# Kernel optimization log

Measured on AMD Instinct MI355X. Metric: run time of the kernel, lower is better.

Reference implementation:

```python
import jax, jax.numpy as jnp
import numpy as np

D_MODEL = 1024
NUM_HEAD = 16
D_K = D_MODEL // NUM_HEAD


def setup_inputs() -> dict:
    key = jax.random.key(0)
    ks = jax.random.split(key, 9)
    s = 1.0 / np.sqrt(D_MODEL)
    x = jax.random.normal(ks[0], (2, 2048, D_MODEL), dtype=jnp.float32)
    Wq = jax.random.uniform(ks[1], (D_MODEL, D_MODEL), jnp.float32, -s, s)
    bq = jax.random.uniform(ks[2], (D_MODEL,), jnp.float32, -s, s)
    Wk = jax.random.uniform(ks[3], (D_MODEL, D_MODEL), jnp.float32, -s, s)
    bk = jax.random.uniform(ks[4], (D_MODEL,), jnp.float32, -s, s)
    Wv = jax.random.uniform(ks[5], (D_MODEL, D_MODEL), jnp.float32, -s, s)
    bv = jax.random.uniform(ks[6], (D_MODEL,), jnp.float32, -s, s)
    Wo = jax.random.uniform(ks[7], (D_MODEL, D_MODEL), jnp.float32, -s, s)
    bo = jax.random.uniform(ks[8], (D_MODEL,), jnp.float32, -s, s)
    return {"x": x, "Wq": Wq, "bq": bq, "Wk": Wk, "bk": bk,
            "Wv": Wv, "bv": bv, "Wo": Wo, "bo": bo}


def reference(x, Wq, bq, Wk, bk, Wv, bv, Wo, bo):
    b, n, d = x.shape
    h, dk = NUM_HEAD, D_K
    # Linear projections (torch Linear: x @ W.T + b)
    q = (x @ Wq.T + bq).reshape(b, n, h, dk).transpose(0, 2, 1, 3)  # [b,h,n,dk]
    k = (x @ Wk.T + bk).reshape(b, n, h, dk).transpose(0, 2, 1, 3)
    v = (x @ Wv.T + bv).reshape(b, n, h, dk).transpose(0, 2, 1, 3)
    scores = jnp.einsum('bhqd,bhkd->bhqk', q, k) / jnp.sqrt(jnp.float32(dk))
    attn = jax.nn.softmax(scores, axis=-1)  # [b,h,n,n]
    out = jnp.einsum('bhqk,bhkd->bhqd', attn, v)
    out = out.transpose(0, 2, 1, 3).reshape(b, n, d)
    return out @ Wo.T + bo
```

## Files before the change

kernel.cpp:

```cpp
#include <hip/hip_runtime.h>

#define BATCH   2
#define SEQ     2048
#define DMODEL  1024
#define NHEAD   16
#define DKH     64
#define MTOT    (BATCH*SEQ)
#define KDIM    DMODEL

#define XB    0u
#define WQB   (4u*1024u*1024u)
#define WKB   (5u*1024u*1024u)
#define WVB   (6u*1024u*1024u)
#define WOB   (7u*1024u*1024u)
#define QOFF  (8u*1024u*1024u)
#define KOFF  (12u*1024u*1024u)
#define VOFF  (16u*1024u*1024u)
#define OOFF  (20u*1024u*1024u)

typedef __bf16 bf16x8 __attribute__((ext_vector_type(8)));
typedef __bf16 bf16x4 __attribute__((ext_vector_type(4)));
typedef float  f32x4  __attribute__((ext_vector_type(4)));
typedef float  f32x16 __attribute__((ext_vector_type(16)));

__device__ __forceinline__ void async16(const __bf16* g, __bf16* l) {
  __builtin_amdgcn_global_load_lds(
      (const __attribute__((address_space(1))) void*)g,
      (__attribute__((address_space(3))) void*)l, 16, 0, 0);
}

#define VWAIT(N) asm volatile("s_waitcnt vmcnt(" #N ")" ::: "memory")

__device__ __forceinline__ unsigned cvtpk_bf16(float lo, float hi) {
  unsigned r;
  asm("v_cvt_pk_bf16_f32 %0, %1, %2" : "=v"(r) : "v"(lo), "v"(hi));
  return r;
}
__device__ __forceinline__ void plswap(unsigned& a, unsigned& b) {
  asm("v_permlane32_swap_b32 %0, %1" : "+v"(a), "+v"(b));
}

__global__ __launch_bounds__(256) void cvt_fp32_bf16(
    const float* __restrict__ x,  const float* __restrict__ wq,
    const float* __restrict__ wk, const float* __restrict__ wv,
    const float* __restrict__ wo, __bf16* __restrict__ ws)
{
  const float* src; __bf16* dst; int n;
  switch (blockIdx.y) {
    case 0:  src = x;  dst = ws + XB;  n = 4 * 1024 * 1024; break;
    case 1:  src = wq; dst = ws + WQB; n = 1024 * 1024;     break;
    case 2:  src = wk; dst = ws + WKB; n = 1024 * 1024;     break;
    case 3:  src = wv; dst = ws + WVB; n = 1024 * 1024;     break;
    default: src = wo; dst = ws + WOB; n = 1024 * 1024;     break;
  }
  const int i = (blockIdx.x * 256 + threadIdx.x) * 8;
  if (i < n) {
    const float4 a = *(const float4*)(src + i);
    const float4 b = *(const float4*)(src + i + 4);
    bf16x8 o;
    o[0] = (__bf16)a.x; o[1] = (__bf16)a.y; o[2] = (__bf16)a.z; o[3] = (__bf16)a.w;
    o[4] = (__bf16)b.x; o[5] = (__bf16)b.y; o[6] = (__bf16)b.z; o[7] = (__bf16)b.w;
    *(bf16x8*)(dst + i) = o;
  }
}

__device__ __forceinline__ void gemm_stage128(
    const __bf16* __restrict__ A, const __bf16* __restrict__ W,
    int m0, int n0, int kt, __bf16* slot, int w, int lane)
{
#pragma unroll
  for (int issue = 0; issue < 2; ++issue) {
    const int cbase = issue * 256 + (w << 6);
    const int c     = cbase + lane;
    const int row   = c >> 2;
    const int goff  = ((c & 3) ^ (row & 3)) << 3;
    async16(A + (size_t)(m0 + row) * KDIM + kt + goff, slot + cbase * 8);
    async16(W + (size_t)(n0 + row) * KDIM + kt + goff, slot + 4096 + cbase * 8);
  }
}

__device__ __forceinline__ void gemm_step128(
    const __bf16* slot, int wr, int wc, int ln15, int quad, f32x4 (&acc)[4][4])
{
  const __bf16* A_lds = slot;
  const __bf16* B_lds = slot + 4096;
  bf16x8 af[4], bfr[4];
#pragma unroll
  for (int i = 0; i < 4; ++i) {
    const int row = wr + i * 16 + ln15;
    af[i] = *(const bf16x8*)&A_lds[row * 32 + ((quad ^ (row & 3)) << 3)];
  }
#pragma unroll
  for (int j = 0; j < 4; ++j) {
    const int row = wc + j * 16 + ln15;
    bfr[j] = *(const bf16x8*)&B_lds[row * 32 + ((quad ^ (row & 3)) << 3)];
  }
#pragma unroll
  for (int i = 0; i < 4; ++i)
#pragma unroll
    for (int j = 0; j < 4; ++j)
      acc[i][j] = __builtin_amdgcn_mfma_f32_16x16x32_bf16(af[i], bfr[j], acc[i][j], 0, 0, 0);
}

__device__ __forceinline__ void gemm128_core(
    const __bf16* __restrict__ A, const __bf16* __restrict__ W,
    int m0, int n0, __bf16* lds, f32x4 (&acc)[4][4])
{
  const int t    = threadIdx.x;
  const int w    = t >> 6;
  const int lane = t & 63;
  const int ln15 = lane & 15;
  const int quad = lane >> 4;
  const int wr   = (w >> 1) << 6;
  const int wc   = (w & 1) << 6;

#pragma unroll
  for (int i = 0; i < 4; ++i)
#pragma unroll
    for (int j = 0; j < 4; ++j) acc[i][j] = (f32x4){0.f, 0.f, 0.f, 0.f};

  __bf16* s0 = lds;
  __bf16* s1 = lds + 8192;
  __bf16* s2 = lds + 16384;

  gemm_stage128(A, W, m0, n0, 0,  s0, w, lane);
  gemm_stage128(A, W, m0, n0, 32, s1, w, lane);

  int kt = 0;
#pragma unroll 1
  for (int i3 = 0; i3 < 10; ++i3) {
    VWAIT(4); __builtin_amdgcn_s_barrier();
    gemm_stage128(A, W, m0, n0, kt + 64, s2, w, lane);
    gemm_step128(s0, wr, wc, ln15, quad, acc);

    VWAIT(4); __builtin_amdgcn_s_barrier();
    gemm_stage128(A, W, m0, n0, kt + 96, s0, w, lane);
    gemm_step128(s1, wr, wc, ln15, quad, acc);

    VWAIT(4); __builtin_amdgcn_s_barrier();
    gemm_stage128(A, W, m0, n0, kt + 128, s1, w, lane);
    gemm_step128(s2, wr, wc, ln15, quad, acc);
    kt += 96;
  }
  VWAIT(4); __builtin_amdgcn_s_barrier();
  gemm_step128(s0, wr, wc, ln15, quad, acc);
  VWAIT(0); __builtin_amdgcn_s_barrier();
  gemm_step128(s1, wr, wc, ln15, quad, acc);
}

__global__ __launch_bounds__(256) void qkv_gemm(
    const __bf16* __restrict__ X,
    const __bf16* __restrict__ Wq, const float* __restrict__ bq,
    const __bf16* __restrict__ Wk, const float* __restrict__ bk,
    const __bf16* __restrict__ Wv, const float* __restrict__ bv,
    __bf16* __restrict__ ws)
{
  __shared__ __align__(16) __bf16 lds[24576];

  const int z = blockIdx.z;
  const __bf16* W    = (z == 0) ? Wq : (z == 1) ? Wk : Wv;
  const float*  bias = (z == 0) ? bq : (z == 1) ? bk : bv;
  __bf16* out = ws + ((z == 0) ? QOFF : (z == 1) ? KOFF : VOFF);
  const float scale = (z == 0) ? 0.125f * 1.44269504088896f : 1.0f;

  const int m0 = blockIdx.x * 128;
  const int n0 = blockIdx.y * 128;

  f32x4 acc[4][4];
  gemm128_core(X, W, m0, n0, lds, acc);

  const int t = threadIdx.x, w = t >> 6, lane = t & 63;
  const int ln15 = lane & 15, quad = lane >> 4;
  const int wr = (w >> 1) << 6, wc = (w & 1) << 6;

  float bj4[4];
#pragma unroll
  for (int j = 0; j < 4; ++j) bj4[j] = bias[n0 + wc + j * 16 + ln15];

  __syncthreads();
  __bf16* scr = lds + (w << 10);

  const int bb = m0 >> 11;
  const int s_base = (m0 & 2047) + wr;
  const int h = (n0 + wc) >> 6;

  if (z != 2) {
    const int rdrow = lane & 15, rdseg = lane >> 4;
#pragma unroll
    for (int i = 0; i < 4; ++i) {
#pragma unroll
      for (int j = 0; j < 4; ++j)
#pragma unroll
        for (int rr = 0; rr < 4; ++rr)
          scr[(quad * 4 + rr) * 64 + j * 16 + ln15] =
              (__bf16)((acc[i][j][rr] + bj4[j]) * scale);
      bf16x8 v0 = *(const bf16x8*)&scr[rdrow * 64 + rdseg * 16];
      bf16x8 v1 = *(const bf16x8*)&scr[rdrow * 64 + rdseg * 16 + 8];
      const int s = s_base + i * 16 + rdrow;
      __bf16* p = out + (((size_t)(bb * NHEAD + h)) * SEQ + s) * DKH + rdseg * 16;
      *(bf16x8*)p = v0;
      *(bf16x8*)&p[8] = v1;
    }
  } else {
#pragma unroll
    for (int i = 0; i < 4; ++i) {
#pragma unroll
      for (int j = 0; j < 4; ++j) {
        bf16x4 pk;
#pragma unroll
        for (int rr = 0; rr < 4; ++rr) pk[rr] = (__bf16)(acc[i][j][rr] + bj4[j]);
        *(bf16x4*)&scr[(j * 16 + ln15) * 16 + quad * 4] = pk;
      }
      bf16x8 c0 = *(const bf16x8*)&scr[lane * 16];
      bf16x8 c1 = *(const bf16x8*)&scr[lane * 16 + 8];
      __bf16* p = out + (((size_t)(bb * NHEAD + h)) * DKH + lane) * SEQ
                      + s_base + i * 16;
      *(bf16x8*)p = c0;
      *(bf16x8*)&p[8] = c1;
    }
  }
}

__device__ __forceinline__ void out_stage(
    const __bf16* __restrict__ A, const __bf16* __restrict__ Wo,
    int m0, int n0, int kt, __bf16* slot, int w, int lane)
{
  {
    const int c = (w << 6) + lane;
    const int row = c >> 2;
    const int goff = ((c & 3) ^ (row & 3)) << 3;
    async16(A + (size_t)(m0 + row) * KDIM + kt + goff, slot + c * 8);
  }
#pragma unroll
  for (int issue = 0; issue < 2; ++issue) {
    const int cbase = issue * 256 + (w << 6);
    const int c = cbase + lane;
    const int row = c >> 2;
    const int goff = ((c & 3) ^ (row & 3)) << 3;
    async16(Wo + (size_t)(n0 + row) * KDIM + kt + goff, slot + 2048 + cbase * 8);
  }
}

__device__ __forceinline__ void out_step(
    const __bf16* slot, int w, int ln15, int quad, f32x4 (&acc)[4][2])
{
  const __bf16* A_lds = slot;
  const __bf16* B_lds = slot + 2048;
  bf16x8 af[4], bfr[2];
#pragma unroll
  for (int i = 0; i < 4; ++i) {
    const int row = i * 16 + ln15;
    af[i] = *(const bf16x8*)&A_lds[row * 32 + ((quad ^ (row & 3)) << 3)];
  }
#pragma unroll
  for (int j = 0; j < 2; ++j) {
    const int row = (w << 5) + j * 16 + ln15;
    bfr[j] = *(const bf16x8*)&B_lds[row * 32 + ((quad ^ (row & 3)) << 3)];
  }
#pragma unroll
  for (int i = 0; i < 4; ++i)
#pragma unroll
    for (int j = 0; j < 2; ++j)
      acc[i][j] = __builtin_amdgcn_mfma_f32_16x16x32_bf16(af[i], bfr[j], acc[i][j], 0, 0, 0);
}

__global__ __launch_bounds__(256) void out_gemm(
    const __bf16* __restrict__ A, const __bf16* __restrict__ Wo,
    const float* __restrict__ bo, float* __restrict__ out)
{
  __shared__ __align__(16) __bf16 lds[18432];

  const int m0 = blockIdx.x * 64;
  const int n0 = blockIdx.y * 128;

  const int t = threadIdx.x, w = t >> 6, lane = t & 63;
  const int ln15 = lane & 15, quad = lane >> 4;

  f32x4 acc[4][2];
#pragma unroll
  for (int i = 0; i < 4; ++i)
#pragma unroll
    for (int j = 0; j < 2; ++j) acc[i][j] = (f32x4){0.f, 0.f, 0.f, 0.f};

  __bf16* s0 = lds;
  __bf16* s1 = lds + 6144;
  __bf16* s2 = lds + 12288;

  out_stage(A, Wo, m0, n0, 0,  s0, w, lane);
  out_stage(A, Wo, m0, n0, 32, s1, w, lane);

  int kt = 0;
#pragma unroll 1
  for (int i3 = 0; i3 < 10; ++i3) {
    VWAIT(3); __builtin_amdgcn_s_barrier();
    out_stage(A, Wo, m0, n0, kt + 64, s2, w, lane);
    out_step(s0, w, ln15, quad, acc);

    VWAIT(3); __builtin_amdgcn_s_barrier();
    out_stage(A, Wo, m0, n0, kt + 96, s0, w, lane);
    out_step(s1, w, ln15, quad, acc);

    VWAIT(3); __builtin_amdgcn_s_barrier();
    out_stage(A, Wo, m0, n0, kt + 128, s1, w, lane);
    out_step(s2, w, ln15, quad, acc);
    kt += 96;
  }
  VWAIT(3); __builtin_amdgcn_s_barrier();
  out_step(s0, w, ln15, quad, acc);
  VWAIT(0); __builtin_amdgcn_s_barrier();
  out_step(s1, w, ln15, quad, acc);

  float bj2[2];
#pragma unroll
  for (int j = 0; j < 2; ++j) bj2[j] = bo[n0 + (w << 5) + j * 16 + ln15];

  __syncthreads();
  float* scrf = (float*)lds + (w << 9);

  const int rdrow = lane & 15, rdseg = lane >> 4;
#pragma unroll
  for (int i = 0; i < 4; ++i) {
#pragma unroll
    for (int j = 0; j < 2; ++j) {
      f32x4 v;
#pragma unroll
      for (int rr = 0; rr < 4; ++rr) v[rr] = acc[i][j][rr] + bj2[j];
      *(f32x4*)&scrf[(j * 16 + ln15) * 16 + quad * 4] = v;
    }
    const int m = m0 + i * 16 + rdrow;
    float* p = out + (size_t)m * DMODEL + n0 + (w << 5) + rdseg * 8;
#pragma unroll
    for (int cc = 0; cc < 2; ++cc) {
      f32x4 v;
#pragma unroll
      for (int e = 0; e < 4; ++e)
        v[e] = scrf[(rdseg * 8 + cc * 4 + e) * 16 + rdrow];
      *(f32x4*)&p[cc * 4] = v;
    }
  }
}

__device__ __forceinline__ void softmax_frag(const f32x16& s, float& l,
                                             bf16x8& pfa, bf16x8& pfb)
{
  float p[16];
#pragma unroll
  for (int r = 0; r < 16; ++r) {
    p[r] = __builtin_amdgcn_exp2f(s[r]);
    l += p[r];
  }
  unsigned A0 = cvtpk_bf16(p[0],  p[1]);
  unsigned A1 = cvtpk_bf16(p[2],  p[3]);
  unsigned B0 = cvtpk_bf16(p[4],  p[5]);
  unsigned B1 = cvtpk_bf16(p[6],  p[7]);
  unsigned C0 = cvtpk_bf16(p[8],  p[9]);
  unsigned C1 = cvtpk_bf16(p[10], p[11]);
  unsigned D0 = cvtpk_bf16(p[12], p[13]);
  unsigned D1 = cvtpk_bf16(p[14], p[15]);
  plswap(A0, B0);
  plswap(A1, B1);
  plswap(C0, D0);
  plswap(C1, D1);
  union { unsigned u[4]; bf16x8 v; } ua, ub;
  ua.u[0] = A0; ua.u[1] = A1; ua.u[2] = B0; ua.u[3] = B1;
  ub.u[0] = C0; ub.u[1] = C1; ub.u[2] = D0; ub.u[3] = D1;
  pfa = ua.v;
  pfb = ub.v;
}

__device__ __forceinline__ void pvstep(const __bf16* Vs, int kh, int KS, int hl,
                                       int ln31, const bf16x8& PF,
                                       f32x16& o0, f32x16& o1)
{
  const int vchunk = (kh << 3) + 2 * KS + hl;
  bf16x8 vf0 = *(const bf16x8*)&Vs[ln31 * 128 + ((vchunk ^ (ln31 & 15)) << 3)];
  bf16x8 vf1 = *(const bf16x8*)&Vs[(32 + ln31) * 128 +
                                   ((vchunk ^ ((32 + ln31) & 15)) << 3)];
  o0 = __builtin_amdgcn_mfma_f32_32x32x16_bf16(PF, vf0, o0, 0, 0, 0);
  o1 = __builtin_amdgcn_mfma_f32_32x32x16_bf16(PF, vf1, o1, 0, 0, 0);
}

__device__ __forceinline__ void attn_tile_compute(
    const __bf16* Ks, const __bf16* Vs, const bf16x8 (&qf)[4],
    int kh, int ln31, int hl, float& l_lane, f32x16& o0, f32x16& o1)
{
#pragma unroll
  for (int half = 0; half < 2; ++half) {
    f32x16 s;
#pragma unroll
    for (int r = 0; r < 16; ++r) s[r] = 0.f;
    const int kr = (kh << 6) + half * 32 + ln31;
    __builtin_amdgcn_s_setprio(1);
#pragma unroll
    for (int ks = 0; ks < 4; ++ks) {
      bf16x8 kf = *(const bf16x8*)&Ks[kr * 64 + (((2 * ks + hl) ^ (kr & 7)) << 3)];
      s = __builtin_amdgcn_mfma_f32_32x32x16_bf16(kf, qf[ks], s, 0, 0, 0);
    }
    __builtin_amdgcn_s_setprio(0);
    bf16x8 pa, pb;
    softmax_frag(s, l_lane, pa, pb);
    __builtin_amdgcn_s_setprio(1);
    pvstep(Vs, kh, half * 2 + 0, hl, ln31, pa, o0, o1);
    pvstep(Vs, kh, half * 2 + 1, hl, ln31, pb, o0, o1);
    __builtin_amdgcn_s_setprio(0);
  }
}

__global__ __launch_bounds__(512, 2) void attn_kernel(
    const __bf16* __restrict__ Qb, const __bf16* __restrict__ Kb,
    const __bf16* __restrict__ Vtb, __bf16* __restrict__ Ob)
{
  __shared__ __align__(16) __bf16 smem[3 * 128 * 64];
  __bf16* QP = smem;
  __bf16* Ks = smem + 8192;
  __bf16* Vs = smem + 16384;

  const int t = threadIdx.x, w = t >> 6, lane = t & 63;
  const int ln31 = lane & 31, hl = lane >> 5;
  const int g  = w & 3;
  const int kh = w >> 2;
  const int bh = blockIdx.x;
  const int q0 = blockIdx.y * 128;
  const int bb = bh >> 4, hh = bh & 15;

  const __bf16* Qg = Qb + (size_t)bh * SEQ * DKH + (size_t)q0 * DKH;
  const __bf16* Kg = Kb + (size_t)bh * SEQ * DKH;
  const __bf16* Vg = Vtb + (size_t)bh * DKH * SEQ;

#pragma unroll
  for (int issue = 0; issue < 2; ++issue) {
    const int cbase = issue * 512 + (w << 6);
    const int c = cbase + lane;
    const int row = c >> 3;
    const int goff = ((c & 7) ^ (row & 7)) << 3;
    async16(Qg + (size_t)row * DKH + goff, QP + cbase * 8);
  }

  const int c0 = t, c1 = t + 512;
  const int krow0 = c0 >> 3; const int kgo0 = ((c0 & 7) ^ (krow0 & 7)) << 3;
  const int krow1 = c1 >> 3; const int kgo1 = ((c1 & 7) ^ (krow1 & 7)) << 3;
  const int vrow0 = c0 >> 4; const int vgo0 = ((c0 & 15) ^ (vrow0 & 15)) << 3;
  const int vrow1 = c1 >> 4; const int vgo1 = ((c1 & 15) ^ (vrow1 & 15)) << 3;
  const __bf16* kp0 = Kg + (size_t)krow0 * DKH + kgo0;
  const __bf16* kp1 = Kg + (size_t)krow1 * DKH + kgo1;
  const __bf16* vp0 = Vg + (size_t)vrow0 * SEQ + vgo0;
  const __bf16* vp1 = Vg + (size_t)vrow1 * SEQ + vgo1;
  __bf16* kd0 = Ks + c0 * 8;  __bf16* kd1 = Ks + c1 * 8;
  __bf16* vd0 = Vs + c0 * 8;  __bf16* vd1 = Vs + c1 * 8;

  bf16x8 krg0 = *(const bf16x8*)kp0;
  bf16x8 krg1 = *(const bf16x8*)kp1;
  bf16x8 vrg0 = *(const bf16x8*)vp0;
  bf16x8 vrg1 = *(const bf16x8*)vp1;

  __syncthreads();

  const int qrow = (g << 5) + ln31;
  bf16x8 qf[4];
#pragma unroll
  for (int ks = 0; ks < 4; ++ks) {
    const int chunk = ((2 * ks + hl) ^ (qrow & 7));
    qf[ks] = *(const bf16x8*)&QP[qrow * 64 + (chunk << 3)];
  }

  float l_lane = 0.f;
  f32x16 o0, o1;
#pragma unroll
  for (int r = 0; r < 16; ++r) { o0[r] = 0.f; o1[r] = 0.f; }

  for (int kt = 0; kt < SEQ; kt += 128) {
    __syncthreads();
    *(bf16x8*)kd0 = krg0;  *(bf16x8*)kd1 = krg1;
    *(bf16x8*)vd0 = vrg0;  *(bf16x8*)vd1 = vrg1;
    __syncthreads();
    if (kt + 128 < SEQ) {
      krg0 = *(const bf16x8*)(kp0 + (size_t)(kt + 128) * DKH);
      krg1 = *(const bf16x8*)(kp1 + (size_t)(kt + 128) * DKH);
      vrg0 = *(const bf16x8*)(vp0 + kt + 128);
      vrg1 = *(const bf16x8*)(vp1 + kt + 128);
    }
    attn_tile_compute(Ks, Vs, qf, kh, ln31, hl, l_lane, o0, o1);
  }

  __syncthreads();
  float* cmb = (float*)smem;
  const int dsw = ln31 & 7;
  l_lane += __shfl_xor(l_lane, 32);

  if (w >= 4) {
    float* base = cmb + (g << 11);
#pragma unroll
    for (int gg = 0; gg < 4; ++gg) {
      const int qq = ((2 * gg + hl) ^ dsw) << 2;
      f32x4 va, vb;
#pragma unroll
      for (int rr = 0; rr < 4; ++rr) { va[rr] = o0[4 * gg + rr]; vb[rr] = o1[4 * gg + rr]; }
      *(f32x4*)&base[ln31 * 32 + qq]        = va;
      *(f32x4*)&base[(32 + ln31) * 32 + qq] = vb;
    }
    if (hl == 0) cmb[8192 + (g << 5) + ln31] = l_lane;
  }
  __syncthreads();
  if (w < 4) {
    float* base = cmb + (g << 11);
#pragma unroll
    for (int gg = 0; gg < 4; ++gg) {
      const int qq = ((2 * gg + hl) ^ dsw) << 2;
      const f32x4 va = *(const f32x4*)&base[ln31 * 32 + qq];
      const f32x4 vb = *(const f32x4*)&base[(32 + ln31) * 32 + qq];
#pragma unroll
      for (int rr = 0; rr < 4; ++rr) { o0[4 * gg + rr] += va[rr]; o1[4 * gg + rr] += vb[rr]; }
    }
    const float inv = 1.0f / (l_lane + cmb[8192 + (g << 5) + ln31]);

#pragma unroll
    for (int r = 0; r < 16; ++r) {
      const int qi = (r & 3) + 8 * (r >> 2) + 4 * hl;
      const float iq = __shfl(inv, qi);
      const int q = q0 + (g << 5) + qi;
      __bf16* rowp = Ob + ((size_t)(bb * SEQ + q)) * DMODEL + hh * DKH;
      rowp[ln31]      = (__bf16)(o0[r] * iq);
      rowp[32 + ln31] = (__bf16)(o1[r] * iq);
    }
  }
}

extern "C" void kernel_launch(void* const* d_in, const int* in_sizes, int n_in,
                              void* d_out, int out_size, void* d_ws, size_t ws_size,
                              hipStream_t stream)
{
  const float* x  = (const float*)d_in[0];
  const float* Wq = (const float*)d_in[1];
  const float* bq = (const float*)d_in[2];
  const float* Wk = (const float*)d_in[3];
  const float* bk = (const float*)d_in[4];
  const float* Wv = (const float*)d_in[5];
  const float* bv = (const float*)d_in[6];
  const float* Wo = (const float*)d_in[7];
  const float* bo = (const float*)d_in[8];
  float*  out = (float*)d_out;
  __bf16* ws  = (__bf16*)d_ws;

  cvt_fp32_bf16<<<dim3(2048, 5, 1), 256, 0, stream>>>(x, Wq, Wk, Wv, Wo, ws);

  qkv_gemm<<<dim3(MTOT / 128, DMODEL / 128, 3), 256, 0, stream>>>(
      ws + XB, ws + WQB, bq, ws + WKB, bk, ws + WVB, bv, ws);

  attn_kernel<<<dim3(BATCH * NHEAD, SEQ / 128), 512, 0, stream>>>(
      ws + QOFF, ws + KOFF, ws + VOFF, ws + OOFF);

  out_gemm<<<dim3(MTOT / 64, DMODEL / 128), 256, 0, stream>>>(
      ws + OOFF, ws + WOB, bo, out);
}
```

Measured before the change: 182.5 us.

## Double-buffer K/V tiles in LDS with async global-to-LDS loads

Replaces the register-staged K/V prefetch, which needed an LDS store and two full syncthreads per tile, with direct async global-to-LDS copies into two ping-pong K/V buffers driven by vmcnt waits and raw barriers. Tile loads for step j+2 are issued while tile j+1 is computed, which is meant to hide global latency and cut per-tile register pressure and synchronisation. LDS use grows from 48KB to 80KB per block, and the launch-bounds hint is raised to 4 blocks per unit even though that LDS footprint likely caps real occupancy well below 4 and may restrict registers.

```diff
diff --git a/kernel.cpp b/kernel.cpp
--- a/kernel.cpp
+++ b/kernel.cpp
@@ -406,14 +406,16 @@
   }
 }
 
-__global__ __launch_bounds__(512, 2) void attn_kernel(
+__global__ __launch_bounds__(512, 4) void attn_kernel(
     const __bf16* __restrict__ Qb, const __bf16* __restrict__ Kb,
     const __bf16* __restrict__ Vtb, __bf16* __restrict__ Ob)
 {
-  __shared__ __align__(16) __bf16 smem[3 * 128 * 64];
+  __shared__ __align__(16) __bf16 smem[5 * 128 * 64];
   __bf16* QP = smem;
-  __bf16* Ks = smem + 8192;
-  __bf16* Vs = smem + 16384;
+  __bf16* K0 = smem + 8192;
+  __bf16* V0 = smem + 16384;
+  __bf16* K1 = smem + 24576;
+  __bf16* V1 = smem + 32768;
 
   const int t = threadIdx.x, w = t >> 6, lane = t & 63;
   const int ln31 = lane & 31, hl = lane >> 5;
@@ -427,6 +429,20 @@
   const __bf16* Kg = Kb + (size_t)bh * SEQ * DKH;
   const __bf16* Vg = Vtb + (size_t)bh * DKH * SEQ;
 
+  auto stage_kv = [&](int kt, __bf16* Ks, __bf16* Vs) {
+#pragma unroll
+    for (int issue = 0; issue < 2; ++issue) {
+      const int cbase = issue * 512 + (w << 6);
+      const int c = cbase + lane;
+      const int krow = c >> 3;
+      const int kgoff = ((c & 7) ^ (krow & 7)) << 3;
+      async16(Kg + (size_t)(kt + krow) * DKH + kgoff, Ks + cbase * 8);
+      const int vrow = c >> 4;
+      const int vgoff = ((c & 15) ^ (vrow & 15)) << 3;
+      async16(Vg + (size_t)vrow * SEQ + kt + vgoff, Vs + cbase * 8);
+    }
+  };
+
 #pragma unroll
   for (int issue = 0; issue < 2; ++issue) {
     const int cbase = issue * 512 + (w << 6);
@@ -435,25 +451,11 @@
     const int goff = ((c & 7) ^ (row & 7)) << 3;
     async16(Qg + (size_t)row * DKH + goff, QP + cbase * 8);
   }
-
-  const int c0 = t, c1 = t + 512;
-  const int krow0 = c0 >> 3; const int kgo0 = ((c0 & 7) ^ (krow0 & 7)) << 3;
-  const int krow1 = c1 >> 3; const int kgo1 = ((c1 & 7) ^ (krow1 & 7)) << 3;
-  const int vrow0 = c0 >> 4; const int vgo0 = ((c0 & 15) ^ (vrow0 & 15)) << 3;
-  const int vrow1 = c1 >> 4; const int vgo1 = ((c1 & 15) ^ (vrow1 & 15)) << 3;
-  const __bf16* kp0 = Kg + (size_t)krow0 * DKH + kgo0;
-  const __bf16* kp1 = Kg + (size_t)krow1 * DKH + kgo1;
-  const __bf16* vp0 = Vg + (size_t)vrow0 * SEQ + vgo0;
-  const __bf16* vp1 = Vg + (size_t)vrow1 * SEQ + vgo1;
-  __bf16* kd0 = Ks + c0 * 8;  __bf16* kd1 = Ks + c1 * 8;
-  __bf16* vd0 = Vs + c0 * 8;  __bf16* vd1 = Vs + c1 * 8;
-
-  bf16x8 krg0 = *(const bf16x8*)kp0;
-  bf16x8 krg1 = *(const bf16x8*)kp1;
-  bf16x8 vrg0 = *(const bf16x8*)vp0;
-  bf16x8 vrg1 = *(const bf16x8*)vp1;
-
-  __syncthreads();
+  stage_kv(0, K0, V0);
+  stage_kv(128, K1, V1);
+
+  VWAIT(8);
+  __builtin_amdgcn_s_barrier();
 
   const int qrow = (g << 5) + ln31;
   bf16x8 qf[4];
@@ -468,19 +470,22 @@
 #pragma unroll
   for (int r = 0; r < 16; ++r) { o0[r] = 0.f; o1[r] = 0.f; }
 
-  for (int kt = 0; kt < SEQ; kt += 128) {
-    __syncthreads();
-    *(bf16x8*)kd0 = krg0;  *(bf16x8*)kd1 = krg1;
-    *(bf16x8*)vd0 = vrg0;  *(bf16x8*)vd1 = vrg1;
-    __syncthreads();
-    if (kt + 128 < SEQ) {
-      krg0 = *(const bf16x8*)(kp0 + (size_t)(kt + 128) * DKH);
-      krg1 = *(const bf16x8*)(kp1 + (size_t)(kt + 128) * DKH);
-      vrg0 = *(const bf16x8*)(vp0 + kt + 128);
-      vrg1 = *(const bf16x8*)(vp1 + kt + 128);
-    }
-    attn_tile_compute(Ks, Vs, qf, kh, ln31, hl, l_lane, o0, o1);
-  }
+#pragma unroll 1
+  for (int j = 0; j < 14; j += 2) {
+    VWAIT(4); __builtin_amdgcn_s_barrier();
+    attn_tile_compute(K0, V0, qf, kh, ln31, hl, l_lane, o0, o1);
+    __builtin_amdgcn_s_barrier();
+    stage_kv((j + 2) * 128, K0, V0);
+
+    VWAIT(4); __builtin_amdgcn_s_barrier();
+    attn_tile_compute(K1, V1, qf, kh, ln31, hl, l_lane, o0, o1);
+    __builtin_amdgcn_s_barrier();
+    stage_kv((j + 3) * 128, K1, V1);
+  }
+  VWAIT(4); __builtin_amdgcn_s_barrier();
+  attn_tile_compute(K0, V0, qf, kh, ln31, hl, l_lane, o0, o1);
+  VWAIT(0); __builtin_amdgcn_s_barrier();
+  attn_tile_compute(K1, V1, qf, kh, ln31, hl, l_lane, o0, o1);
 
   __syncthreads();
   float* cmb = (float*)smem;
```

Result: no change. 182.9 us (+0.2%).
